# Kernel optimization log

Measured on AMD Instinct MI355X. Metric: run time of the kernel, lower is better.

## Reference

```python
import jax, jax.numpy as jnp
import numpy as np

N_NODES = 100000
N_EDGES = 1250000
IN_F = 64
HID = 64
N_CLS = 1

def _xavier(key, shape, gain):
    fan_in, fan_out = shape[1], shape[0]
    a = gain * np.sqrt(6.0 / (fan_in + fan_out))
    return jax.random.uniform(key, shape, jnp.float32, -a, a)

def setup_inputs() -> dict:
    key = jax.random.key(0)
    ks = jax.random.split(key, 8)
    x = jax.random.normal(ks[0], (N_NODES, IN_F), jnp.float32)
    e = jax.random.normal(ks[1], (N_EDGES, IN_F), jnp.float32)
    src = jax.random.randint(ks[2], (N_EDGES,), 0, N_NODES, jnp.int64 if jax.config.jax_enable_x64 else jnp.int32)
    dst = jax.random.randint(ks[3], (N_EDGES,), 0, N_NODES, jnp.int64 if jax.config.jax_enable_x64 else jnp.int32)
    W1 = _xavier(ks[4], (IN_F, 3 * IN_F), 0.1)
    b1 = jnp.zeros((IN_F,), jnp.float32)
    W2 = _xavier(ks[5], (HID, IN_F), 0.1)
    b2 = jnp.zeros((HID,), jnp.float32)
    W3 = _xavier(ks[6], (N_CLS, HID), 0.01)
    class_ratio = 0.1
    b3 = jnp.full((N_CLS,), -np.log((1 - class_ratio) / class_ratio), jnp.float32)
    return {"x": x, "e": e, "src": src, "dst": dst,
            "W1": W1, "b1": b1, "W2": W2, "b2": b2, "W3": W3, "b3": b3}

def reference(x, e, src, dst, W1, b1, W2, b2, W3, b3):
    # gather src/dst node features, concat with edge feats: [E, 3*IN_F]
    data = jnp.concatenate((x[src], x[dst], e), axis=1)
    h = jax.nn.relu(data @ W1.T + b1)      # [E, IN_F]  (dropout p=0.0 -> identity)
    h = jax.nn.relu(h @ W2.T + b2)         # [E, HID]
    score = h @ W3.T + b3                  # [E, N_CLS]
    return score
```

## Files before the change

kernel.cpp:

```cpp
#include <hip/hip_runtime.h>

typedef unsigned short u16;
typedef __bf16 bf16x8 __attribute__((ext_vector_type(8)));
typedef float f32x4 __attribute__((ext_vector_type(4)));

#define EBLK 64

__device__ __forceinline__ float bf2f(u16 u) {
    union { unsigned i; float f; } v; v.i = ((unsigned)u) << 16; return v.f;
}
__device__ __forceinline__ u16 f2bf(float f) {
    unsigned u = __float_as_uint(f);
    return (u16)((u + 0x7FFFu + ((u >> 16) & 1u)) >> 16);
}

__device__ __forceinline__ uint4 load_gran(const char* rowp, int g, bool bf) {
    if (bf) return ((const uint4*)rowp)[g];
    const float4* p = (const float4*)rowp + g * 2;
    float4 a = p[0], b = p[1];
    union { u16 h[8]; uint4 u; } r;
    r.h[0] = f2bf(a.x); r.h[1] = f2bf(a.y); r.h[2] = f2bf(a.z); r.h[3] = f2bf(a.w);
    r.h[4] = f2bf(b.x); r.h[5] = f2bf(b.y); r.h[6] = f2bf(b.z); r.h[7] = f2bf(b.w);
    return r.u;
}
__device__ __forceinline__ float ldf(const void* p, int i, bool bf) {
    return bf ? bf2f(((const u16*)p)[i]) : ((const float*)p)[i];
}
__device__ __forceinline__ long getidx(const void* p, long i, bool i64) {
    return i64 ? (long)((const long long*)p)[i] : (long)((const int*)p)[i];
}

__global__ __launch_bounds__(256) void sp_kernel(
    const void* __restrict__ xv,
    const void* __restrict__ ev,
    const void* __restrict__ srcv,
    const void* __restrict__ dstv,
    const void* __restrict__ W1v,
    const void* __restrict__ b1v,
    const void* __restrict__ W2v,
    const void* __restrict__ b2v,
    const void* __restrict__ W3v,
    const void* __restrict__ b3v,
    void* __restrict__ outv,
    int E, int ntiles)
{
    const u16 tb3 = *(const u16*)b3v;
    const bool BF = ((tb3 & 0xFF80) == 0xC000);
    const int* s32 = (const int*)srcv;
    const bool I64 = ((s32[1] | s32[3] | s32[5] | s32[7]) == 0);
    const long xrb = BF ? 128 : 256;

    __shared__ __align__(16) char sData[EBLK * 384];
    __shared__ __align__(16) char sW1[64 * 384];
    __shared__ __align__(16) char sW2[64 * 128];
    __shared__ __align__(16) char sH1[EBLK * 128];
    __shared__ float sB1[64], sB2[64], sW3v[64];

    const int tid = threadIdx.x;
    const int row = tid >> 2, q = tid & 3;
    const int rswz = (row & 7) << 4;
    const float b3f = ldf(b3v, 0, BF);

    {
        const char* w1r = (const char*)W1v + (long)row * (BF ? 384 : 768);
        #pragma unroll
        for (int i = 0; i < 6; ++i) {
            int g = q + 4 * i;
            *(uint4*)(sW1 + row * 384 + ((g * 16) ^ rswz)) = load_gran(w1r, g, BF);
        }
        const char* w2r = (const char*)W2v + (long)row * xrb;
        #pragma unroll
        for (int i = 0; i < 2; ++i) {
            int g = q + 4 * i;
            *(uint4*)(sW2 + row * 128 + ((g * 16) ^ rswz)) = load_gran(w2r, g, BF);
        }
        if (tid < 64) {
            sB1[tid] = ldf(b1v, tid, BF);
            sB2[tid] = ldf(b2v, tid, BF);
            sW3v[tid] = ldf(W3v, tid, BF);
        }
    }
    __syncthreads();

    const int wave = tid >> 6, lane = tid & 63;
    const int lr = lane & 15;
    const int lg = lane >> 4;
    const f32x4 z4 = {0.f, 0.f, 0.f, 0.f};
    const char* xb = (const char*)xv;
    const char* eb = (const char*)ev;

    for (int tile = blockIdx.x; tile < ntiles; tile += gridDim.x) {
        const long base = (long)tile * EBLK;

        {
            long ei = base + row; if (ei >= E) ei = E - 1;
            const char* ps = xb + getidx(srcv, ei, I64) * xrb;
            const char* pd = xb + getidx(dstv, ei, I64) * xrb;
            const char* pe = eb + ei * xrb;
            #pragma unroll
            for (int i = 0; i < 2; ++i) {
                int g = q + 4 * i;
                *(uint4*)(sData + row * 384 + ((g * 16) ^ rswz)) = load_gran(ps, g, BF);
                *(uint4*)(sData + row * 384 + ((128 + g * 16) ^ rswz)) = load_gran(pd, g, BF);
                *(uint4*)(sData + row * 384 + ((256 + g * 16) ^ rswz)) = load_gran(pe, g, BF);
            }
        }
        __syncthreads();

        bf16x8 a[6];
        {
            const int r = wave * 16 + lr, swz = (r & 7) << 4;
            #pragma unroll
            for (int kt = 0; kt < 6; ++kt)
                a[kt] = *(const bf16x8*)(sData + r * 384 + ((kt * 64 + lg * 16) ^ swz));
        }
        f32x4 acc[4] = {z4, z4, z4, z4};
        #pragma unroll
        for (int nt = 0; nt < 4; ++nt) {
            const int wr = nt * 16 + lr, swz = (wr & 7) << 4;
            #pragma unroll
            for (int kt = 0; kt < 6; ++kt) {
                bf16x8 b = *(const bf16x8*)(sW1 + wr * 384 + ((kt * 64 + lg * 16) ^ swz));
                acc[nt] = __builtin_amdgcn_mfma_f32_16x16x32_bf16(a[kt], b, acc[nt], 0, 0, 0);
            }
        }
        #pragma unroll
        for (int nt = 0; nt < 4; ++nt) {
            const int col = nt * 16 + lr;
            const float bias = sB1[col];
            #pragma unroll
            for (int r = 0; r < 4; ++r) {
                const int hr = wave * 16 + lg * 4 + r;
                float v = acc[nt][r] + bias;
                v = v > 0.f ? v : 0.f;
                *(u16*)(sH1 + hr * 128 + ((col * 2) ^ ((hr & 7) << 4))) = f2bf(v);
            }
        }
        __syncthreads();

        bf16x8 a2[2];
        {
            const int r = wave * 16 + lr, swz = (r & 7) << 4;
            #pragma unroll
            for (int kt = 0; kt < 2; ++kt)
                a2[kt] = *(const bf16x8*)(sH1 + r * 128 + ((kt * 64 + lg * 16) ^ swz));
        }
        f32x4 acc2[4] = {z4, z4, z4, z4};
        #pragma unroll
        for (int nt = 0; nt < 4; ++nt) {
            const int wr = nt * 16 + lr, swz = (wr & 7) << 4;
            #pragma unroll
            for (int kt = 0; kt < 2; ++kt) {
                bf16x8 b = *(const bf16x8*)(sW2 + wr * 128 + ((kt * 64 + lg * 16) ^ swz));
                acc2[nt] = __builtin_amdgcn_mfma_f32_16x16x32_bf16(a2[kt], b, acc2[nt], 0, 0, 0);
            }
        }

        float sacc[4] = {0.f, 0.f, 0.f, 0.f};
        #pragma unroll
        for (int nt = 0; nt < 4; ++nt) {
            const int col = nt * 16 + lr;
            const float w3c = sW3v[col], bias = sB2[col];
            #pragma unroll
            for (int r = 0; r < 4; ++r) {
                float v = acc2[nt][r] + bias;
                v = v > 0.f ? v : 0.f;
                sacc[r] += v * w3c;
            }
        }
        #pragma unroll
        for (int m = 1; m < 16; m <<= 1) {
            #pragma unroll
            for (int r = 0; r < 4; ++r)
                sacc[r] += __shfl_xor(sacc[r], m, 64);
        }

        if (lr == 0) {
            long e0 = base + wave * 16 + lg * 4;
            float v0 = b3f + sacc[0], v1 = b3f + sacc[1];
            float v2 = b3f + sacc[2], v3 = b3f + sacc[3];
            if (e0 + 4 <= E) {
                if (BF) {
                    ushort4 pk = { f2bf(v0), f2bf(v1), f2bf(v2), f2bf(v3) };
                    *(ushort4*)((u16*)outv + e0) = pk;
                } else {
                    float4 pk = { v0, v1, v2, v3 };
                    *(float4*)((float*)outv + e0) = pk;
                }
            } else if (e0 < E) {
                float vv[4] = {v0, v1, v2, v3};
                for (int j = 0; j < 4 && e0 + j < E; ++j) {
                    if (BF) ((u16*)outv)[e0 + j] = f2bf(vv[j]);
                    else    ((float*)outv)[e0 + j] = vv[j];
                }
            }
        }
        __syncthreads();
    }
}

extern "C" void kernel_launch(void* const* d_in, const int* in_sizes, int n_in,
                              void* d_out, int out_size, void* d_ws, size_t ws_size,
                              hipStream_t stream) {
    const int E = in_sizes[2];
    const int ntiles = (E + EBLK - 1) / EBLK;
    const int grid = ntiles < 4096 ? ntiles : 4096;
    sp_kernel<<<grid, 256, 0, stream>>>(
        d_in[0], d_in[1], d_in[2], d_in[3], d_in[4], d_in[5],
        d_in[6], d_in[7], d_in[8], d_in[9], d_out, E, ntiles);
}
```

Baseline: 249.6 us.

## Make each wave own 16-edge tiles, gather directly into registers, prefetch indices

Each wave now processes its own 16-edge tile independently. Node and edge features are gathered from global memory straight into MFMA A-operand registers instead of being staged through shared memory, and the src/dst indices for the next tile are prefetched. W2, the biases and W3 now live in registers, and the block-wide barriers are replaced by a wave-local LDS wait. The aim is to remove block-wide synchronisation and LDS staging so gathers overlap with compute. The cost is higher register pressure under launch_bounds(256,4), and the grid is capped at 1024 blocks.

```diff
diff --git a/kernel.cpp b/kernel.cpp
--- a/kernel.cpp
+++ b/kernel.cpp
@@ -1,10 +1,9 @@
 #include <hip/hip_runtime.h>
 
 typedef unsigned short u16;
+typedef __bf16 bf16;
 typedef __bf16 bf16x8 __attribute__((ext_vector_type(8)));
 typedef float f32x4 __attribute__((ext_vector_type(4)));
-
-#define EBLK 64
 
 __device__ __forceinline__ float bf2f(u16 u) {
     union { unsigned i; float f; } v; v.i = ((unsigned)u) << 16; return v.f;
@@ -13,15 +12,16 @@
     unsigned u = __float_as_uint(f);
     return (u16)((u + 0x7FFFu + ((u >> 16) & 1u)) >> 16);
 }
-
-__device__ __forceinline__ uint4 load_gran(const char* rowp, int g, bool bf) {
-    if (bf) return ((const uint4*)rowp)[g];
+__device__ __forceinline__ bf16x8 cvt8(float4 a, float4 b) {
+    bf16x8 r;
+    r[0] = (bf16)a.x; r[1] = (bf16)a.y; r[2] = (bf16)a.z; r[3] = (bf16)a.w;
+    r[4] = (bf16)b.x; r[5] = (bf16)b.y; r[6] = (bf16)b.z; r[7] = (bf16)b.w;
+    return r;
+}
+__device__ __forceinline__ bf16x8 ldg8(const char* rowp, int g, bool bf) {
+    if (bf) return ((const bf16x8*)rowp)[g];
     const float4* p = (const float4*)rowp + g * 2;
-    float4 a = p[0], b = p[1];
-    union { u16 h[8]; uint4 u; } r;
-    r.h[0] = f2bf(a.x); r.h[1] = f2bf(a.y); r.h[2] = f2bf(a.z); r.h[3] = f2bf(a.w);
-    r.h[4] = f2bf(b.x); r.h[5] = f2bf(b.y); r.h[6] = f2bf(b.z); r.h[7] = f2bf(b.w);
-    return r.u;
+    return cvt8(p[0], p[1]);
 }
 __device__ __forceinline__ float ldf(const void* p, int i, bool bf) {
     return bf ? bf2f(((const u16*)p)[i]) : ((const float*)p)[i];
@@ -30,7 +30,7 @@
     return i64 ? (long)((const long long*)p)[i] : (long)((const int*)p)[i];
 }
 
-__global__ __launch_bounds__(256) void sp_kernel(
+__global__ __launch_bounds__(256, 4) void sp_kernel(
     const void* __restrict__ xv,
     const void* __restrict__ ev,
     const void* __restrict__ srcv,
@@ -42,7 +42,7 @@
     const void* __restrict__ W3v,
     const void* __restrict__ b3v,
     void* __restrict__ outv,
-    int E, int ntiles)
+    int E, long nwt)
 {
     const u16 tb3 = *(const u16*)b3v;
     const bool BF = ((tb3 & 0xFF80) == 0xC000);
@@ -50,34 +50,20 @@
     const bool I64 = ((s32[1] | s32[3] | s32[5] | s32[7]) == 0);
     const long xrb = BF ? 128 : 256;
 
-    __shared__ __align__(16) char sData[EBLK * 384];
     __shared__ __align__(16) char sW1[64 * 384];
-    __shared__ __align__(16) char sW2[64 * 128];
-    __shared__ __align__(16) char sH1[EBLK * 128];
-    __shared__ float sB1[64], sB2[64], sW3v[64];
+    __shared__ __align__(16) char sH1[64 * 128];
 
     const int tid = threadIdx.x;
-    const int row = tid >> 2, q = tid & 3;
-    const int rswz = (row & 7) << 4;
-    const float b3f = ldf(b3v, 0, BF);
 
     {
+        const int row = tid >> 2, q = tid & 3;
+        const int rswz = (row & 7) << 4;
         const char* w1r = (const char*)W1v + (long)row * (BF ? 384 : 768);
         #pragma unroll
         for (int i = 0; i < 6; ++i) {
             int g = q + 4 * i;
-            *(uint4*)(sW1 + row * 384 + ((g * 16) ^ rswz)) = load_gran(w1r, g, BF);
-        }
-        const char* w2r = (const char*)W2v + (long)row * xrb;
-        #pragma unroll
-        for (int i = 0; i < 2; ++i) {
-            int g = q + 4 * i;
-            *(uint4*)(sW2 + row * 128 + ((g * 16) ^ rswz)) = load_gran(w2r, g, BF);
-        }
-        if (tid < 64) {
-            sB1[tid] = ldf(b1v, tid, BF);
-            sB2[tid] = ldf(b2v, tid, BF);
-            sW3v[tid] = ldf(W3v, tid, BF);
+            bf16x8 v = ldg8(w1r, g, BF);
+            *(bf16x8*)(sW1 + row * 384 + ((g * 16) ^ rswz)) = v;
         }
     }
     __syncthreads();
@@ -85,35 +71,60 @@
     const int wave = tid >> 6, lane = tid & 63;
     const int lr = lane & 15;
     const int lg = lane >> 4;
-    const f32x4 z4 = {0.f, 0.f, 0.f, 0.f};
+
+    bf16x8 w2f[2][4];
+    float bias1[4], bias2[4], w3c[4];
+    #pragma unroll
+    for (int nt = 0; nt < 4; ++nt) {
+        const int c = nt * 16 + lr;
+        const char* w2r = (const char*)W2v + (long)c * xrb;
+        #pragma unroll
+        for (int kt = 0; kt < 2; ++kt)
+            w2f[kt][nt] = ldg8(w2r, kt * 4 + lg, BF);
+        bias1[nt] = ldf(b1v, c, BF);
+        bias2[nt] = ldf(b2v, c, BF);
+        w3c[nt]   = ldf(W3v, c, BF);
+    }
+    const float b3f = ldf(b3v, 0, BF);
+
     const char* xb = (const char*)xv;
     const char* eb = (const char*)ev;
-
-    for (int tile = blockIdx.x; tile < ntiles; tile += gridDim.x) {
-        const long base = (long)tile * EBLK;
+    const f32x4 z4 = {0.f, 0.f, 0.f, 0.f};
+
+    const long wid = (long)blockIdx.x * 4 + wave;
+    const long nw  = (long)gridDim.x * 4;
+
+    long t = wid, s = 0, d = 0;
+    if (t < nwt) {
+        long ei = t * 16 + lr; if (ei >= E) ei = E - 1;
+        s = getidx(srcv, ei, I64);
+        d = getidx(dstv, ei, I64);
+    }
+
+    for (; t < nwt; t += nw) {
+        const long base = t * 16;
+        long ei = base + lr; if (ei >= E) ei = E - 1;
+        const char* ps = xb + s * xrb;
+        const char* pd = xb + d * xrb;
+        const char* pe = eb + ei * xrb;
+
+        bf16x8 a[6];
+        #pragma unroll
+        for (int kt = 0; kt < 2; ++kt) {
+            a[kt]     = ldg8(ps, kt * 4 + lg, BF);
+            a[2 + kt] = ldg8(pd, kt * 4 + lg, BF);
+            a[4 + kt] = ldg8(pe, kt * 4 + lg, BF);
+        }
 
         {
-            long ei = base + row; if (ei >= E) ei = E - 1;
-            const char* ps = xb + getidx(srcv, ei, I64) * xrb;
-            const char* pd = xb + getidx(dstv, ei, I64) * xrb;
-            const char* pe = eb + ei * xrb;
-            #pragma unroll
-            for (int i = 0; i < 2; ++i) {
-                int g = q + 4 * i;
-                *(uint4*)(sData + row * 384 + ((g * 16) ^ rswz)) = load_gran(ps, g, BF);
-                *(uint4*)(sData + row * 384 + ((128 + g * 16) ^ rswz)) = load_gran(pd, g, BF);
-                *(uint4*)(sData + row * 384 + ((256 + g * 16) ^ rswz)) = load_gran(pe, g, BF);
-            }
-        }
-        __syncthreads();
-
-        bf16x8 a[6];
-        {
-            const int r = wave * 16 + lr, swz = (r & 7) << 4;
-            #pragma unroll
-            for (int kt = 0; kt < 6; ++kt)
-                a[kt] = *(const bf16x8*)(sData + r * 384 + ((kt * 64 + lg * 16) ^ swz));
-        }
+            long tn = t + nw;
+            if (tn < nwt) {
+                long ein = tn * 16 + lr; if (ein >= E) ein = E - 1;
+                s = getidx(srcv, ein, I64);
+                d = getidx(dstv, ein, I64);
+            }
+        }
+
         f32x4 acc[4] = {z4, z4, z4, z4};
         #pragma unroll
         for (int nt = 0; nt < 4; ++nt) {
@@ -124,10 +135,11 @@
                 acc[nt] = __builtin_amdgcn_mfma_f32_16x16x32_bf16(a[kt], b, acc[nt], 0, 0, 0);
             }
         }
+
         #pragma unroll
         for (int nt = 0; nt < 4; ++nt) {
             const int col = nt * 16 + lr;
-            const float bias = sB1[col];
+            const float bias = bias1[nt];
             #pragma unroll
             for (int r = 0; r < 4; ++r) {
                 const int hr = wave * 16 + lg * 4 + r;
@@ -136,7 +148,8 @@
                 *(u16*)(sH1 + hr * 128 + ((col * 2) ^ ((hr & 7) << 4))) = f2bf(v);
             }
         }
-        __syncthreads();
+        asm volatile("s_waitcnt lgkmcnt(0)" ::: "memory");
+        __builtin_amdgcn_sched_barrier(0);
 
         bf16x8 a2[2];
         {
@@ -148,24 +161,19 @@
         f32x4 acc2[4] = {z4, z4, z4, z4};
         #pragma unroll
         for (int nt = 0; nt < 4; ++nt) {
-            const int wr = nt * 16 + lr, swz = (wr & 7) << 4;
-            #pragma unroll
-            for (int kt = 0; kt < 2; ++kt) {
-                bf16x8 b = *(const bf16x8*)(sW2 + wr * 128 + ((kt * 64 + lg * 16) ^ swz));
-                acc2[nt] = __builtin_amdgcn_mfma_f32_16x16x32_bf16(a2[kt], b, acc2[nt], 0, 0, 0);
-            }
+            #pragma unroll
+            for (int kt = 0; kt < 2; ++kt)
+                acc2[nt] = __builtin_amdgcn_mfma_f32_16x16x32_bf16(a2[kt], w2f[kt][nt], acc2[nt], 0, 0, 0);
         }
 
         float sacc[4] = {0.f, 0.f, 0.f, 0.f};
         #pragma unroll
         for (int nt = 0; nt < 4; ++nt) {
-            const int col = nt * 16 + lr;
-            const float w3c = sW3v[col], bias = sB2[col];
             #pragma unroll
             for (int r = 0; r < 4; ++r) {
-                float v = acc2[nt][r] + bias;
+                float v = acc2[nt][r] + bias2[nt];
                 v = v > 0.f ? v : 0.f;
-                sacc[r] += v * w3c;
+                sacc[r] += v * w3c[nt];
             }
         }
         #pragma unroll
@@ -176,7 +184,7 @@
         }
 
         if (lr == 0) {
-            long e0 = base + wave * 16 + lg * 4;
+            long e0 = base + lg * 4;
             float v0 = b3f + sacc[0], v1 = b3f + sacc[1];
             float v2 = b3f + sacc[2], v3 = b3f + sacc[3];
             if (e0 + 4 <= E) {
@@ -195,7 +203,6 @@
                 }
             }
         }
-        __syncthreads();
     }
 }
 
@@ -203,9 +210,10 @@
                               void* d_out, int out_size, void* d_ws, size_t ws_size,
                               hipStream_t stream) {
     const int E = in_sizes[2];
-    const int ntiles = (E + EBLK - 1) / EBLK;
-    const int grid = ntiles < 4096 ? ntiles : 4096;
-    sp_kernel<<<grid, 256, 0, stream>>>(
+    const long nwt = (E + 15) / 16;
+    long blocks = (nwt + 3) / 4;
+    if (blocks > 1024) blocks = 1024;
+    sp_kernel<<<(int)blocks, 256, 0, stream>>>(
         d_in[0], d_in[1], d_in[2], d_in[3], d_in[4], d_in[5],
-        d_in[6], d_in[7], d_in[8], d_in[9], d_out, E, ntiles);
-}
+        d_in[6], d_in[7], d_in[8], d_in[9], d_out, E, nwt);
+}
```

Result: faster. 200.3 us (-19.7%).
